# Optimization experiments

Measured on AMD Instinct MI355X. Metric: run time of the kernel, lower is better.

Reference implementation:

```python
import jax, jax.numpy as jnp
import numpy as np
from jax import lax

# Config (matches init_kwargs)
E = 8         # num_routed_experts
K = 2         # topk
D = 2048      # d_model
H = 1408      # moe_hidden_dimension
NS = 2        # num_shared_experts
B, T = 2, 2048
EPS = 1e-20   # topk_norm_epsilon
HS = H * NS   # shared expert hidden dim


def setup_inputs() -> dict:
    key = jax.random.key(0)
    ks = jax.random.split(key, 8)
    s = 0.02
    return {
        "x": jax.random.normal(ks[0], (B, T, D), jnp.float32),
        "router_w": jax.random.normal(ks[1], (E, D), jnp.float32) * 0.006,
        # routed experts, stacked: gate/up: [E, D, H], down: [E, H, D]
        "wg": jax.random.normal(ks[2], (E, D, H), jnp.float32) * s,
        "wu": jax.random.normal(ks[3], (E, D, H), jnp.float32) * s,
        "wd": jax.random.normal(ks[4], (E, H, D), jnp.float32) * s,
        # shared expert (single big SwiGLU FFN)
        "sg": jax.random.normal(ks[5], (D, HS), jnp.float32) * s,
        "su": jax.random.normal(ks[6], (D, HS), jnp.float32) * s,
        "sd": jax.random.normal(ks[7], (HS, D), jnp.float32) * s,
    }


def _silu(v):
    return v * jax.nn.sigmoid(v)


def reference(x, router_w, wg, wu, wd, sg, su, sd):
    b, t, d = x.shape
    xf = x.reshape(b * t, d)                       # [N, D]
    n = xf.shape[0]

    # Router: softmax over experts, then top-k masking (DeepSeek style)
    gates = jax.nn.softmax(xf @ router_w.T, axis=-1)           # [N, E]
    topv, topi = lax.top_k(gates, K)                           # [N, K]
    masked = jnp.zeros_like(gates).at[jnp.arange(n)[:, None], topi].set(topv)
    # normalized_moe_gates=True
    masked = masked / (masked.sum(axis=-1, keepdims=True) + EPS)  # [N, E]

    # Per-expert SwiGLU FFN, weighted-accumulated over experts.
    # Mathematically identical to gather/grouped-GEMM/scatter-add combine:
    # tokens with zero gate for expert e contribute 0.
    def step(acc, p):
        wg_e, wu_e, wd_e, g_e = p                  # g_e: [N] gate weights
        y = (_silu(xf @ wg_e) * (xf @ wu_e)) @ wd_e  # [N, D]
        return acc + y * g_e[:, None], None

    routed, _ = lax.scan(step, jnp.zeros_like(xf), (wg, wu, wd, masked.T))

    # Shared experts (dense path applied to every token)
    shared = (_silu(xf @ sg) * (xf @ su)) @ sd      # [N, D]

    return (routed + shared).reshape(b, t, d)
```

## Files before the change

kernel.cpp:

```cpp
#include <hip/hip_runtime.h>
#include <hip/hip_bf16.h>
#include <cstdint>

#define NTOK 4096
#define DMODEL 2048
#define NEXP 8
#define HR 1408
#define HSHARED 2816
#define MAXT64 136
#define MAXT128 72

typedef __attribute__((ext_vector_type(8))) short bf16x8;
typedef __attribute__((ext_vector_type(4))) float f32x4;

__device__ inline unsigned short f2b(float f) {
    unsigned u = __float_as_uint(f);
    u += 0x7fffu + ((u >> 16) & 1u);
    return (unsigned short)(u >> 16);
}
__device__ inline unsigned pack2(float a, float b) {
    return (unsigned)f2b(a) | ((unsigned)f2b(b) << 16);
}

__device__ __forceinline__ void gll16(unsigned short* lds, const unsigned short* g) {
    __builtin_amdgcn_global_load_lds(
        (__attribute__((address_space(1))) void*)g,
        (__attribute__((address_space(3))) void*)lds, 16, 0, 0);
}

__global__ __launch_bounds__(256) void k_router(const float* __restrict__ x,
                                                const float* __restrict__ rw,
                                                int* __restrict__ topi,
                                                float* __restrict__ topw,
                                                int* __restrict__ counts) {
    int gw = (blockIdx.x * 256 + threadIdx.x) >> 6;
    int lane = threadIdx.x & 63;
    if (gw >= NTOK) return;
    const float* xr = x + (size_t)gw * DMODEL;
    float s[NEXP] = {0.f,0.f,0.f,0.f,0.f,0.f,0.f,0.f};
    for (int d = lane; d < DMODEL; d += 64) {
        float xv = xr[d];
#pragma unroll
        for (int e = 0; e < NEXP; e++) s[e] = fmaf(xv, rw[e * DMODEL + d], s[e]);
    }
#pragma unroll
    for (int e = 0; e < NEXP; e++)
        for (int o = 32; o > 0; o >>= 1) s[e] += __shfl_xor(s[e], o, 64);
    if (lane == 0) {
        int i1 = 0;
#pragma unroll
        for (int e = 1; e < NEXP; e++) if (s[e] > s[i1]) i1 = e;
        int i2 = (i1 == 0) ? 1 : 0;
#pragma unroll
        for (int e = 0; e < NEXP; e++) if (e != i1 && s[e] > s[i2]) i2 = e;
        float mx = s[0];
#pragma unroll
        for (int e = 1; e < NEXP; e++) mx = fmaxf(mx, s[e]);
        float den = 0.f, ex[NEXP];
#pragma unroll
        for (int e = 0; e < NEXP; e++) { ex[e] = __expf(s[e] - mx); den += ex[e]; }
        float v1 = ex[i1] / den, v2 = ex[i2] / den;
        float inv = 1.f / (v1 + v2 + 1e-20f);
        topi[2 * gw] = i1; topi[2 * gw + 1] = i2;
        topw[2 * gw] = v1 * inv; topw[2 * gw + 1] = v2 * inv;
        atomicAdd(&counts[i1], 1); atomicAdd(&counts[i2], 1);
    }
}

__global__ void k_scan(int* counts, int* offsets, int* cursors, int* ntiles,
                       int* tile_e, int* tile_r, int step) {
    if (threadIdx.x == 0 && blockIdx.x == 0) {
        int off = 0, nt = 0;
        for (int e = 0; e < NEXP; e++) {
            offsets[e] = off; cursors[e] = off;
            int c = counts[e];
            for (int r = 0; r < c; r += step) { tile_e[nt] = e; tile_r[nt] = r; nt++; }
            off += c;
        }
        ntiles[0] = nt;
    }
}

__global__ __launch_bounds__(256) void k_fill(const int* __restrict__ topi,
                                              const float* __restrict__ topw,
                                              int* cursors, int* at, float* aw) {
    int t = blockIdx.x * 256 + threadIdx.x;
    if (t >= NTOK) return;
#pragma unroll
    for (int k = 0; k < 2; k++) {
        int e = topi[2 * t + k];
        int pos = atomicAdd(&cursors[e], 1);
        at[pos] = t; aw[pos] = topw[2 * t + k];
    }
}

__global__ __launch_bounds__(256) void k_cvt_x(const float* __restrict__ src,
                                               unsigned short* __restrict__ dst) {
    size_t i = ((size_t)blockIdx.x * 256 + threadIdx.x) * 8;
    float4 a = *(const float4*)(src + i);
    float4 b = *(const float4*)(src + i + 4);
    uint4 v; v.x = pack2(a.x, a.y); v.y = pack2(a.z, a.w);
    v.z = pack2(b.x, b.y); v.w = pack2(b.z, b.w);
    *(uint4*)(dst + i) = v;
}

__global__ __launch_bounds__(256) void k_tcvt(const float* __restrict__ src,
                                              unsigned short* __restrict__ dst,
                                              int K, int N) {
    src += (size_t)blockIdx.z * K * N;
    dst += (size_t)blockIdx.z * K * N;
    int n0 = blockIdx.x * 64, k0 = blockIdx.y * 64;
    __shared__ unsigned short T[64][72];
    int t = threadIdx.x;
    int kr = t >> 4, nc = (t & 15) * 4;
#pragma unroll
    for (int i = 0; i < 4; i++) {
        int k = kr + i * 16;
        float4 v = *(const float4*)(src + (size_t)(k0 + k) * N + n0 + nc);
        T[k][nc] = f2b(v.x); T[k][nc + 1] = f2b(v.y);
        T[k][nc + 2] = f2b(v.z); T[k][nc + 3] = f2b(v.w);
    }
    __syncthreads();
    int nr = t >> 3, kc = (t & 7) * 8;
#pragma unroll
    for (int j = 0; j < 2; j++) {
        int n = nr + j * 32;
        unsigned short tmp[8];
#pragma unroll
        for (int u = 0; u < 8; u++) tmp[u] = T[kc + u][n];
        *(uint4*)(dst + (size_t)(n0 + n) * K + k0 + kc) = *(uint4*)tmp;
    }
}


template <bool GATHERED>
__global__ __launch_bounds__(256) void kf_gateup(
    const unsigned short* __restrict__ xb, const unsigned short* __restrict__ BgT,
    const unsigned short* __restrict__ BuT, int K, int Hld, int ebase,
    const int* __restrict__ tile_e, const int* __restrict__ tile_r,
    const int* __restrict__ offsets, const int* __restrict__ counts,
    const int* __restrict__ ntiles, const int* __restrict__ at,
    unsigned short* __restrict__ hout) {
    int m0, mcnt;
    const unsigned short* bgw = BgT;
    const unsigned short* buw = BuT;
    if (GATHERED) {
        if ((int)blockIdx.x >= ntiles[0]) return;
        int e = tile_e[blockIdx.x];
        if (e < ebase || e >= ebase + 4) return;
        int ro = tile_r[blockIdx.x];
        m0 = offsets[e] + ro;
        mcnt = counts[e] - ro; if (mcnt > 128) mcnt = 128;
        size_t wofs = (size_t)(e - ebase) * Hld * K;
        bgw += wofs; buw += wofs;
    } else { m0 = blockIdx.x * 128; mcnt = 128; }
    int n0 = blockIdx.y * 64;

    __shared__ __align__(16) unsigned short As[128 * 64];
    __shared__ __align__(16) unsigned short Bgs[64 * 64];
    __shared__ __align__(16) unsigned short Bus[64 * 64];

    int tid = threadIdx.x;
    int wv = tid >> 6, lane = tid & 63;
    int rbase = tid >> 3;
    int kc = (tid & 7) ^ ((tid >> 3) & 7);
    const unsigned short* arp[4];
#pragma unroll
    for (int j = 0; j < 4; j++) {
        int row = j * 32 + rbase;
        int cl = row < mcnt ? row : mcnt - 1;
        int grow = GATHERED ? at[m0 + cl] : (m0 + cl);
        arp[j] = xb + (size_t)grow * K + kc * 8;
    }
    const unsigned short* bgp[2];
    const unsigned short* bup[2];
#pragma unroll
    for (int j = 0; j < 2; j++) {
        int row = j * 32 + rbase;
        bgp[j] = bgw + (size_t)(n0 + row) * K + kc * 8;
        bup[j] = buw + (size_t)(n0 + row) * K + kc * 8;
    }
    unsigned short* a_l = As + (wv << 6) * 8;
    unsigned short* g_l = Bgs + (wv << 6) * 8;
    unsigned short* u_l = Bus + (wv << 6) * 8;

    int fr = lane & 15, quad = lane >> 4, sw = fr & 7;
    int wm = (wv & 1) << 6, wn = (wv >> 1) << 5;

    f32x4 accg[4][2] = {};
    f32x4 accu[4][2] = {};

    for (int k0 = 0; k0 < K; k0 += 64) {
        __syncthreads();
#pragma unroll
        for (int j = 0; j < 4; j++) gll16(a_l + j * 2048, arp[j] + k0);
#pragma unroll
        for (int j = 0; j < 2; j++) {
            gll16(g_l + j * 2048, bgp[j] + k0);
            gll16(u_l + j * 2048, bup[j] + k0);
        }
        __syncthreads();
#pragma unroll
        for (int s = 0; s < 2; s++) {
            int off = (((s << 2) + quad) ^ sw) << 3;
            bf16x8 a[4], g[2], u[2];
#pragma unroll
            for (int tm = 0; tm < 4; tm++)
                a[tm] = *(const bf16x8*)&As[(wm + tm * 16 + fr) * 64 + off];
#pragma unroll
            for (int tn = 0; tn < 2; tn++) {
                int rb = (wn + tn * 16 + fr) * 64 + off;
                g[tn] = *(const bf16x8*)&Bgs[rb];
                u[tn] = *(const bf16x8*)&Bus[rb];
            }
#pragma unroll
            for (int tm = 0; tm < 4; tm++)
#pragma unroll
                for (int tn = 0; tn < 2; tn++) {
                    accg[tm][tn] = __builtin_amdgcn_mfma_f32_16x16x32_bf16(a[tm], g[tn], accg[tm][tn], 0, 0, 0);
                    accu[tm][tn] = __builtin_amdgcn_mfma_f32_16x16x32_bf16(a[tm], u[tn], accu[tm][tn], 0, 0, 0);
                }
        }
    }
#pragma unroll
    for (int tm = 0; tm < 4; tm++)
#pragma unroll
        for (int r = 0; r < 4; r++) {
            int row = wm + tm * 16 + (quad << 2) + r;
            if (row < mcnt) {
#pragma unroll
                for (int tn = 0; tn < 2; tn++) {
                    float gv = accg[tm][tn][r], uv = accu[tm][tn][r];
                    float hv = (gv / (1.f + __expf(-gv))) * uv;
                    hout[(size_t)(m0 + row) * Hld + n0 + wn + tn * 16 + fr] = f2b(hv);
                }
            }
        }
}

template <bool GATHERED>
__global__ __launch_bounds__(256) void kf_down(
    const unsigned short* __restrict__ h, const unsigned short* __restrict__ BT,
    int K,
    const int* __restrict__ tile_e, const int* __restrict__ tile_r,
    const int* __restrict__ offsets, const int* __restrict__ counts,
    const int* __restrict__ ntiles, const int* __restrict__ at,
    const float* __restrict__ awt, float* __restrict__ out) {
    int m0, mcnt;
    const unsigned short* bw = BT;
    if (GATHERED) {
        if ((int)blockIdx.x >= ntiles[0]) return;
        int e = tile_e[blockIdx.x], ro = tile_r[blockIdx.x];
        m0 = offsets[e] + ro;
        mcnt = counts[e] - ro; if (mcnt > 128) mcnt = 128;
        bw += (size_t)e * DMODEL * K;
    } else { m0 = blockIdx.x * 128; mcnt = 128; }
    int n0 = blockIdx.y * 128;

    __shared__ __align__(16) unsigned short As[128 * 64];
    __shared__ __align__(16) unsigned short Bs[128 * 64];

    int tid = threadIdx.x;
    int wv = tid >> 6, lane = tid & 63;
    int rbase = tid >> 3;
    int kc = (tid & 7) ^ ((tid >> 3) & 7);
    const unsigned short* arp[4];
    const unsigned short* brp[4];
#pragma unroll
    for (int j = 0; j < 4; j++) {
        int row = j * 32 + rbase;
        int cl = row < mcnt ? row : mcnt - 1;
        arp[j] = h + (size_t)(m0 + cl) * K + kc * 8;
        brp[j] = bw + (size_t)(n0 + row) * K + kc * 8;
    }
    unsigned short* a_l = As + (wv << 6) * 8;
    unsigned short* b_l = Bs + (wv << 6) * 8;

    int fr = lane & 15, quad = lane >> 4, sw = fr & 7;
    int wm = (wv & 1) << 6, wn = (wv >> 1) << 6;

    f32x4 acc[4][4] = {};

    for (int k0 = 0; k0 < K; k0 += 64) {
        __syncthreads();
#pragma unroll
        for (int j = 0; j < 4; j++) {
            gll16(a_l + j * 2048, arp[j] + k0);
            gll16(b_l + j * 2048, brp[j] + k0);
        }
        __syncthreads();
#pragma unroll
        for (int s = 0; s < 2; s++) {
            int off = (((s << 2) + quad) ^ sw) << 3;
            bf16x8 a[4], b[4];
#pragma unroll
            for (int tm = 0; tm < 4; tm++)
                a[tm] = *(const bf16x8*)&As[(wm + tm * 16 + fr) * 64 + off];
#pragma unroll
            for (int tn = 0; tn < 4; tn++)
                b[tn] = *(const bf16x8*)&Bs[(wn + tn * 16 + fr) * 64 + off];
#pragma unroll
            for (int tm = 0; tm < 4; tm++)
#pragma unroll
                for (int tn = 0; tn < 4; tn++)
                    acc[tm][tn] = __builtin_amdgcn_mfma_f32_16x16x32_bf16(a[tm], b[tn], acc[tm][tn], 0, 0, 0);
        }
    }
#pragma unroll
    for (int tm = 0; tm < 4; tm++)
#pragma unroll
        for (int r = 0; r < 4; r++) {
            int row = wm + tm * 16 + (quad << 2) + r;
            if (row < mcnt) {
                if (GATHERED) {
                    int tok = at[m0 + row];
                    float w = awt[m0 + row];
#pragma unroll
                    for (int tn = 0; tn < 4; tn++)
                        atomicAdd(&out[(size_t)tok * DMODEL + n0 + wn + tn * 16 + fr],
                                  w * acc[tm][tn][r]);
                } else {
#pragma unroll
                    for (int tn = 0; tn < 4; tn++)
                        out[(size_t)(m0 + row) * DMODEL + n0 + wn + tn * 16 + fr] =
                            acc[tm][tn][r];
                }
            }
        }
}

template <bool GATHERED>
__global__ __launch_bounds__(256) void k_gateup(
    const float* __restrict__ x, const float* __restrict__ Wg,
    const float* __restrict__ Wu, int Hld,
    const int* __restrict__ tile_e, const int* __restrict__ tile_r,
    const int* __restrict__ offsets, const int* __restrict__ counts,
    const int* __restrict__ ntiles, const int* __restrict__ at,
    unsigned short* __restrict__ hout) {
    int m0, mcnt;
    const float* wgp = Wg;
    const float* wup = Wu;
    if (GATHERED) {
        if ((int)blockIdx.x >= ntiles[0]) return;
        int e = tile_e[blockIdx.x], ro = tile_r[blockIdx.x];
        m0 = offsets[e] + ro;
        mcnt = counts[e] - ro; if (mcnt > 64) mcnt = 64;
        size_t wofs = (size_t)e * DMODEL * Hld;
        wgp += wofs; wup += wofs;
    } else { m0 = blockIdx.x * 64; mcnt = 64; }
    int n0 = blockIdx.y * 64;
    __shared__ unsigned short As[64][48];
    __shared__ unsigned short Bgs[64][48];
    __shared__ unsigned short Bus[64][48];
    int tid = threadIdx.x;
    int ai = tid >> 2, ak = (tid & 3) << 3;
    int arowi = m0 + (ai < mcnt ? ai : (mcnt - 1));
    const float* arow = x + (size_t)(GATHERED ? at[arowi] : arowi) * DMODEL;
    int bn = tid >> 2, bk = (tid & 3) << 1;
    const float* bcolg = wgp + (size_t)n0 + bn;
    const float* bcolu = wup + (size_t)n0 + bn;
    int lane = tid & 63, wv = tid >> 6;
    int wm = (wv & 1) << 5, wn = (wv >> 1) << 5;
    int fr = lane & 15, fk = (lane >> 4) << 3;
    f32x4 accg[2][2] = {};
    f32x4 accu[2][2] = {};
    for (int k0 = 0; k0 < DMODEL; k0 += 32) {
        __syncthreads();
        float4 a0 = *(const float4*)(arow + k0 + ak);
        float4 a1 = *(const float4*)(arow + k0 + ak + 4);
        uint4 av; av.x = pack2(a0.x, a0.y); av.y = pack2(a0.z, a0.w);
        av.z = pack2(a1.x, a1.y); av.w = pack2(a1.z, a1.w);
        *(uint4*)&As[ai][ak] = av;
#pragma unroll
        for (int j = 0; j < 4; j++) {
            int kk = bk + (j << 3);
            size_t o0 = (size_t)(k0 + kk) * Hld;
            *(unsigned*)&Bgs[bn][kk] = pack2(bcolg[o0], bcolg[o0 + Hld]);
            *(unsigned*)&Bus[bn][kk] = pack2(bcolu[o0], bcolu[o0 + Hld]);
        }
        __syncthreads();
        bf16x8 af[2], bg[2], bu[2];
#pragma unroll
        for (int t = 0; t < 2; t++) {
            af[t] = *(bf16x8*)&As[wm + t * 16 + fr][fk];
            bg[t] = *(bf16x8*)&Bgs[wn + t * 16 + fr][fk];
            bu[t] = *(bf16x8*)&Bus[wn + t * 16 + fr][fk];
        }
#pragma unroll
        for (int tm = 0; tm < 2; tm++)
#pragma unroll
            for (int tn = 0; tn < 2; tn++) {
                accg[tm][tn] = __builtin_amdgcn_mfma_f32_16x16x32_bf16(af[tm], bg[tn], accg[tm][tn], 0, 0, 0);
                accu[tm][tn] = __builtin_amdgcn_mfma_f32_16x16x32_bf16(af[tm], bu[tn], accu[tm][tn], 0, 0, 0);
            }
    }
    int quad = (lane >> 4) << 2;
#pragma unroll
    for (int tm = 0; tm < 2; tm++)
#pragma unroll
        for (int r = 0; r < 4; r++) {
            int row = wm + tm * 16 + quad + r;
            if (row < mcnt) {
#pragma unroll
                for (int tn = 0; tn < 2; tn++) {
                    float g = accg[tm][tn][r], u = accu[tm][tn][r];
                    float hv = (g / (1.f + __expf(-g))) * u;
                    hout[(size_t)(m0 + row) * Hld + n0 + wn + tn * 16 + fr] = f2b(hv);
                }
            }
        }
}

template <bool GATHERED>
__global__ __launch_bounds__(256) void k_down(
    const unsigned short* __restrict__ h, const float* __restrict__ Wd, int Hld,
    const int* __restrict__ tile_e, const int* __restrict__ tile_r,
    const int* __restrict__ offsets, const int* __restrict__ counts,
    const int* __restrict__ ntiles, const int* __restrict__ at,
    const float* __restrict__ aw, float* __restrict__ out) {
    int m0, mcnt;
    const float* wdp = Wd;
    if (GATHERED) {
        if ((int)blockIdx.x >= ntiles[0]) return;
        int e = tile_e[blockIdx.x], ro = tile_r[blockIdx.x];
        m0 = offsets[e] + ro;
        mcnt = counts[e] - ro; if (mcnt > 64) mcnt = 64;
        wdp += (size_t)e * Hld * DMODEL;
    } else { m0 = blockIdx.x * 64; mcnt = 64; }
    int n0 = blockIdx.y * 64;
    __shared__ unsigned short As[64][48];
    __shared__ unsigned short Bs[64][48];
    int tid = threadIdx.x;
    int ai = tid >> 2, ak = (tid & 3) << 3;
    const unsigned short* arow = h + (size_t)(m0 + (ai < mcnt ? ai : (mcnt - 1))) * Hld;
    int bn = tid >> 2, bk = (tid & 3) << 1;
    const float* bcol = wdp + (size_t)n0 + bn;
    int lane = tid & 63, wv = tid >> 6;
    int wm = (wv & 1) << 5, wn = (wv >> 1) << 5;
    int fr = lane & 15, fk = (lane >> 4) << 3;
    f32x4 acc[2][2] = {};
    for (int k0 = 0; k0 < Hld; k0 += 32) {
        __syncthreads();
        *(uint4*)&As[ai][ak] = *(const uint4*)(arow + k0 + ak);
#pragma unroll
        for (int j = 0; j < 4; j++) {
            int kk = bk + (j << 3);
            size_t o0 = (size_t)(k0 + kk) * DMODEL;
            *(unsigned*)&Bs[bn][kk] = pack2(bcol[o0], bcol[o0 + DMODEL]);
        }
        __syncthreads();
        bf16x8 af[2], bf[2];
#pragma unroll
        for (int t = 0; t < 2; t++) {
            af[t] = *(bf16x8*)&As[wm + t * 16 + fr][fk];
            bf[t] = *(bf16x8*)&Bs[wn + t * 16 + fr][fk];
        }
#pragma unroll
        for (int tm = 0; tm < 2; tm++)
#pragma unroll
            for (int tn = 0; tn < 2; tn++)
                acc[tm][tn] = __builtin_amdgcn_mfma_f32_16x16x32_bf16(af[tm], bf[tn], acc[tm][tn], 0, 0, 0);
    }
    int quad = (lane >> 4) << 2;
#pragma unroll
    for (int tm = 0; tm < 2; tm++)
#pragma unroll
        for (int r = 0; r < 4; r++) {
            int row = wm + tm * 16 + quad + r;
            if (row < mcnt) {
                int mrow = m0 + row;
                int tok = GATHERED ? at[mrow] : mrow;
                float w = GATHERED ? aw[mrow] : 1.f;
#pragma unroll
                for (int tn = 0; tn < 2; tn++)
                    atomicAdd(&out[(size_t)tok * DMODEL + n0 + wn + tn * 16 + fr],
                              w * acc[tm][tn][r]);
            }
        }
}

extern "C" void kernel_launch(void* const* d_in, const int* in_sizes, int n_in,
                              void* d_out, int out_size, void* d_ws, size_t ws_size,
                              hipStream_t stream) {
    (void)in_sizes; (void)n_in;
    const float* x  = (const float*)d_in[0];
    const float* rw = (const float*)d_in[1];
    const float* wg = (const float*)d_in[2];
    const float* wu = (const float*)d_in[3];
    const float* wd = (const float*)d_in[4];
    const float* sg = (const float*)d_in[5];
    const float* su = (const float*)d_in[6];
    const float* sd = (const float*)d_in[7];
    float* out = (float*)d_out;

    int* counts  = (int*)d_ws;
    int* offsets = counts + 8;
    int* cursors = counts + 16;
    int* ntiles  = counts + 24;
    int* tile_e  = counts + 32;
    int* tile_r  = tile_e + 144;
    int* topi    = tile_r + 144;
    float* topw  = (float*)(topi + 8192);
    int* at      = (int*)(topw + 8192);
    float* aw    = (float*)(at + 8192);

    const size_t META = 262144;
    const size_t XB   = (size_t)NTOK * DMODEL * 2;
    const size_t POOL_NEED = 69206016;
    const size_t FAST_NEED = META + XB + POOL_NEED;
    bool fast = ws_size >= FAST_NEED;

    hipMemsetAsync(counts, 0, 32, stream);
    k_router<<<dim3(NTOK / 4), 256, 0, stream>>>(x, rw, topi, topw, counts);
    k_scan<<<1, 64, 0, stream>>>(counts, offsets, cursors, ntiles, tile_e, tile_r,
                                 fast ? 128 : 64);
    k_fill<<<dim3(NTOK / 256), 256, 0, stream>>>(topi, topw, cursors, at, aw);

    if (fast) {
        char* base = (char*)d_ws;
        unsigned short* xb = (unsigned short*)(base + META);
        char* pool = base + META + XB;
        unsigned short* sgT = (unsigned short*)pool;
        unsigned short* suT = (unsigned short*)(pool + 11534336);
        unsigned short* h_s = (unsigned short*)(pool + 23068672);
        unsigned short* sdT = (unsigned short*)(pool + 46137344);
        unsigned short* wgT = (unsigned short*)pool;
        unsigned short* wuT = (unsigned short*)(pool + 23068672);
        unsigned short* h_r = (unsigned short*)(pool + 46137344);
        unsigned short* wdT = (unsigned short*)pool;

        k_cvt_x<<<dim3(4096), 256, 0, stream>>>(x, xb);

        k_tcvt<<<dim3(HSHARED / 64, DMODEL / 64, 1), 256, 0, stream>>>(sg, sgT, DMODEL, HSHARED);
        k_tcvt<<<dim3(HSHARED / 64, DMODEL / 64, 1), 256, 0, stream>>>(su, suT, DMODEL, HSHARED);
        kf_gateup<false><<<dim3(NTOK / 128, HSHARED / 64), 256, 0, stream>>>(
            xb, sgT, suT, DMODEL, HSHARED, 0,
            nullptr, nullptr, nullptr, nullptr, nullptr, nullptr, h_s);
        k_tcvt<<<dim3(DMODEL / 64, HSHARED / 64, 1), 256, 0, stream>>>(sd, sdT, HSHARED, DMODEL);
        kf_down<false><<<dim3(NTOK / 128, DMODEL / 128), 256, 0, stream>>>(
            h_s, sdT, HSHARED,
            nullptr, nullptr, nullptr, nullptr, nullptr, nullptr, nullptr, out);

        k_tcvt<<<dim3(HR / 64, DMODEL / 64, 4), 256, 0, stream>>>(wg, wgT, DMODEL, HR);
        k_tcvt<<<dim3(HR / 64, DMODEL / 64, 4), 256, 0, stream>>>(wu, wuT, DMODEL, HR);
        kf_gateup<true><<<dim3(MAXT128, HR / 64), 256, 0, stream>>>(
            xb, wgT, wuT, DMODEL, HR, 0,
            tile_e, tile_r, offsets, counts, ntiles, at, h_r);
        k_tcvt<<<dim3(HR / 64, DMODEL / 64, 4), 256, 0, stream>>>(
            wg + (size_t)4 * DMODEL * HR, wgT, DMODEL, HR);
        k_tcvt<<<dim3(HR / 64, DMODEL / 64, 4), 256, 0, stream>>>(
            wu + (size_t)4 * DMODEL * HR, wuT, DMODEL, HR);
        kf_gateup<true><<<dim3(MAXT128, HR / 64), 256, 0, stream>>>(
            xb, wgT, wuT, DMODEL, HR, 4,
            tile_e, tile_r, offsets, counts, ntiles, at, h_r);
        k_tcvt<<<dim3(DMODEL / 64, HR / 64, 8), 256, 0, stream>>>(wd, wdT, HR, DMODEL);
        kf_down<true><<<dim3(MAXT128, DMODEL / 128), 256, 0, stream>>>(
            h_r, wdT, HR,
            tile_e, tile_r, offsets, counts, ntiles, at, aw, out);
    } else {
        unsigned short* h_r =
            (unsigned short*)(((uintptr_t)(aw + 8192) + 255) & ~(uintptr_t)255);
        unsigned short* h_s = h_r + (size_t)8192 * HR;
        hipMemsetAsync(out, 0, (size_t)out_size * sizeof(float), stream);
        k_gateup<true><<<dim3(MAXT64, HR / 64), 256, 0, stream>>>(
            x, wg, wu, HR, tile_e, tile_r, offsets, counts, ntiles, at, h_r);
        k_gateup<false><<<dim3(NTOK / 64, HSHARED / 64), 256, 0, stream>>>(
            x, sg, su, HSHARED, nullptr, nullptr, nullptr, nullptr, nullptr, nullptr, h_s);
        k_down<true><<<dim3(MAXT64, DMODEL / 64), 256, 0, stream>>>(
            h_r, wd, HR, tile_e, tile_r, offsets, counts, ntiles, at, aw, out);
        k_down<false><<<dim3(NTOK / 64, DMODEL / 64), 256, 0, stream>>>(
            h_s, sd, HSHARED, nullptr, nullptr, nullptr, nullptr, nullptr, nullptr, nullptr, out);
    }
}
```

Baseline: 965.8 us.

## Merge shared and routed expert GEMMs into single grouped launches, fuse x conversion into router

After: 968.5 us. No clear change (+0.3%).

```diff
diff --git a/kernel.cpp b/kernel.cpp
--- a/kernel.cpp
+++ b/kernel.cpp
@@ -7,7 +7,6 @@
 #define NEXP 8
 #define HR 1408
 #define HSHARED 2816
-#define MAXT64 136
 #define MAXT128 72
 
 typedef __attribute__((ext_vector_type(8))) short bf16x8;
@@ -28,42 +27,60 @@
         (__attribute__((address_space(3))) void*)lds, 16, 0, 0);
 }
 
-__global__ __launch_bounds__(256) void k_router(const float* __restrict__ x,
-                                                const float* __restrict__ rw,
-                                                int* __restrict__ topi,
-                                                float* __restrict__ topw,
-                                                int* __restrict__ counts) {
-    int gw = (blockIdx.x * 256 + threadIdx.x) >> 6;
-    int lane = threadIdx.x & 63;
-    if (gw >= NTOK) return;
-    const float* xr = x + (size_t)gw * DMODEL;
-    float s[NEXP] = {0.f,0.f,0.f,0.f,0.f,0.f,0.f,0.f};
-    for (int d = lane; d < DMODEL; d += 64) {
-        float xv = xr[d];
-#pragma unroll
-        for (int e = 0; e < NEXP; e++) s[e] = fmaf(xv, rw[e * DMODEL + d], s[e]);
-    }
-#pragma unroll
-    for (int e = 0; e < NEXP; e++)
-        for (int o = 32; o > 0; o >>= 1) s[e] += __shfl_xor(s[e], o, 64);
-    if (lane == 0) {
-        int i1 = 0;
-#pragma unroll
-        for (int e = 1; e < NEXP; e++) if (s[e] > s[i1]) i1 = e;
-        int i2 = (i1 == 0) ? 1 : 0;
-#pragma unroll
-        for (int e = 0; e < NEXP; e++) if (e != i1 && s[e] > s[i2]) i2 = e;
-        float mx = s[0];
-#pragma unroll
-        for (int e = 1; e < NEXP; e++) mx = fmaxf(mx, s[e]);
-        float den = 0.f, ex[NEXP];
-#pragma unroll
-        for (int e = 0; e < NEXP; e++) { ex[e] = __expf(s[e] - mx); den += ex[e]; }
-        float v1 = ex[i1] / den, v2 = ex[i2] / den;
-        float inv = 1.f / (v1 + v2 + 1e-20f);
-        topi[2 * gw] = i1; topi[2 * gw + 1] = i2;
-        topw[2 * gw] = v1 * inv; topw[2 * gw + 1] = v2 * inv;
-        atomicAdd(&counts[i1], 1); atomicAdd(&counts[i2], 1);
+__global__ __launch_bounds__(256) void k_router2(const float* __restrict__ x,
+                                                 const float* __restrict__ rw,
+                                                 unsigned short* __restrict__ xb,
+                                                 int* __restrict__ topi,
+                                                 float* __restrict__ topw,
+                                                 int* __restrict__ counts) {
+    __shared__ float rws[NEXP * DMODEL];
+    int tid = threadIdx.x;
+    for (int i = tid * 4; i < NEXP * DMODEL; i += 1024)
+        *(float4*)&rws[i] = *(const float4*)&rw[i];
+    __syncthreads();
+    int wv = tid >> 6, lane = tid & 63;
+#pragma unroll
+    for (int tk = 0; tk < 2; tk++) {
+        int tok = blockIdx.x * 8 + wv * 2 + tk;
+        const float* xr = x + (size_t)tok * DMODEL;
+        unsigned short* xbr = xb + (size_t)tok * DMODEL;
+        float s[NEXP] = {0.f,0.f,0.f,0.f,0.f,0.f,0.f,0.f};
+#pragma unroll
+        for (int i = 0; i < 8; i++) {
+            int d = i * 256 + lane * 4;
+            float4 xv = *(const float4*)(xr + d);
+            uint2 p; p.x = pack2(xv.x, xv.y); p.y = pack2(xv.z, xv.w);
+            *(uint2*)(xbr + d) = p;
+#pragma unroll
+            for (int e = 0; e < NEXP; e++) {
+                float4 w = *(const float4*)&rws[e * DMODEL + d];
+                s[e] = fmaf(xv.x, w.x, s[e]); s[e] = fmaf(xv.y, w.y, s[e]);
+                s[e] = fmaf(xv.z, w.z, s[e]); s[e] = fmaf(xv.w, w.w, s[e]);
+            }
+        }
+#pragma unroll
+        for (int e = 0; e < NEXP; e++)
+#pragma unroll
+            for (int o = 32; o > 0; o >>= 1) s[e] += __shfl_xor(s[e], o, 64);
+        if (lane == 0) {
+            int i1 = 0;
+#pragma unroll
+            for (int e = 1; e < NEXP; e++) if (s[e] > s[i1]) i1 = e;
+            int i2 = (i1 == 0) ? 1 : 0;
+#pragma unroll
+            for (int e = 0; e < NEXP; e++) if (e != i1 && s[e] > s[i2]) i2 = e;
+            float mx = s[0];
+#pragma unroll
+            for (int e = 1; e < NEXP; e++) mx = fmaxf(mx, s[e]);
+            float den = 0.f, ex[NEXP];
+#pragma unroll
+            for (int e = 0; e < NEXP; e++) { ex[e] = __expf(s[e] - mx); den += ex[e]; }
+            float v1 = ex[i1] / den, v2 = ex[i2] / den;
+            float inv = 1.f / (v1 + v2 + 1e-20f);
+            topi[2 * tok] = i1; topi[2 * tok + 1] = i2;
+            topw[2 * tok] = v1 * inv; topw[2 * tok + 1] = v2 * inv;
+            atomicAdd(&counts[i1], 1); atomicAdd(&counts[i2], 1);
+        }
     }
 }
 
@@ -94,22 +111,9 @@
     }
 }
 
-__global__ __launch_bounds__(256) void k_cvt_x(const float* __restrict__ src,
-                                               unsigned short* __restrict__ dst) {
-    size_t i = ((size_t)blockIdx.x * 256 + threadIdx.x) * 8;
-    float4 a = *(const float4*)(src + i);
-    float4 b = *(const float4*)(src + i + 4);
-    uint4 v; v.x = pack2(a.x, a.y); v.y = pack2(a.z, a.w);
-    v.z = pack2(b.x, b.y); v.w = pack2(b.z, b.w);
-    *(uint4*)(dst + i) = v;
-}
-
-__global__ __launch_bounds__(256) void k_tcvt(const float* __restrict__ src,
-                                              unsigned short* __restrict__ dst,
-                                              int K, int N) {
-    src += (size_t)blockIdx.z * K * N;
-    dst += (size_t)blockIdx.z * K * N;
-    int n0 = blockIdx.x * 64, k0 = blockIdx.y * 64;
+__device__ __forceinline__ void tcvt_tile(const float* __restrict__ src,
+                                          unsigned short* __restrict__ dst,
+                                          int N, int dstride, int n0, int k0) {
     __shared__ unsigned short T[64][72];
     int t = threadIdx.x;
     int kr = t >> 4, nc = (t & 15) * 4;
@@ -128,10 +132,259 @@
         unsigned short tmp[8];
 #pragma unroll
         for (int u = 0; u < 8; u++) tmp[u] = T[kc + u][n];
-        *(uint4*)(dst + (size_t)(n0 + n) * K + k0 + kc) = *(uint4*)tmp;
-    }
-}
-
+        *(uint4*)(dst + (size_t)(n0 + n) * dstride + k0 + kc) = *(uint4*)tmp;
+    }
+}
+
+__global__ __launch_bounds__(256) void k_tcvt_gu(const float* __restrict__ wg,
+                                                 const float* __restrict__ wu,
+                                                 unsigned short* __restrict__ wgT,
+                                                 unsigned short* __restrict__ wuT) {
+    int z = blockIdx.z;
+    const float* src = (z < 8 ? wg : wu) + (size_t)(z & 7) * DMODEL * HR;
+    unsigned short* dst = (z < 8 ? wgT : wuT) + (size_t)(z & 7) * HR * DMODEL;
+    tcvt_tile(src, dst, HR, DMODEL, blockIdx.x * 64, blockIdx.y * 64);
+}
+
+__global__ __launch_bounds__(256) void k_tcvt_s(const float* __restrict__ sg,
+                                                const float* __restrict__ su,
+                                                unsigned short* __restrict__ sgT,
+                                                unsigned short* __restrict__ suT) {
+    int z = blockIdx.z;
+    tcvt_tile(z ? su : sg, z ? suT : sgT, HSHARED, DMODEL,
+              blockIdx.x * 64, blockIdx.y * 64);
+}
+
+__global__ __launch_bounds__(256) void k_tcvt_d(const float* __restrict__ wd,
+                                                const float* __restrict__ sd,
+                                                unsigned short* __restrict__ wdT,
+                                                unsigned short* __restrict__ sdT) {
+    int z = blockIdx.z;
+    const float* src;
+    unsigned short* dst;
+    int dstride;
+    if (z < 8) {
+        src = wd + (size_t)z * HR * DMODEL;
+        dst = wdT + (size_t)z * DMODEL * HR;
+        dstride = HR;
+    } else {
+        src = sd + (size_t)(z - 8) * HR * DMODEL;
+        dst = sdT + (size_t)(z - 8) * HR;
+        dstride = HSHARED;
+    }
+    tcvt_tile(src, dst, DMODEL, dstride, blockIdx.x * 64, blockIdx.y * 64);
+}
+
+#define GU_SH_JOBS 1408
+#define GU_RT_NB   22
+__global__ __launch_bounds__(256) void kg_all(
+    const unsigned short* __restrict__ xb,
+    const unsigned short* __restrict__ sgT, const unsigned short* __restrict__ suT,
+    const unsigned short* __restrict__ wgT, const unsigned short* __restrict__ wuT,
+    const int* __restrict__ tile_e, const int* __restrict__ tile_r,
+    const int* __restrict__ offsets, const int* __restrict__ counts,
+    const int* __restrict__ ntiles, const int* __restrict__ at,
+    unsigned short* __restrict__ h_s, unsigned short* __restrict__ h_r) {
+    int j = blockIdx.x;
+    int m0, mcnt, n0, Hld;
+    const unsigned short *Bg, *Bu;
+    unsigned short* ho;
+    bool gath;
+    if (j < GU_SH_JOBS) {
+        gath = false;
+        m0 = (j / 44) * 128; mcnt = 128;
+        n0 = (j % 44) * 64;
+        Bg = sgT; Bu = suT; Hld = HSHARED; ho = h_s;
+    } else {
+        j -= GU_SH_JOBS;
+        int tile = j / GU_RT_NB;
+        if (tile >= ntiles[0]) return;
+        gath = true;
+        n0 = (j % GU_RT_NB) * 64;
+        int e = tile_e[tile], ro = tile_r[tile];
+        m0 = offsets[e] + ro;
+        mcnt = counts[e] - ro; if (mcnt > 128) mcnt = 128;
+        size_t wo = (size_t)e * HR * DMODEL;
+        Bg = wgT + wo; Bu = wuT + wo; Hld = HR; ho = h_r;
+    }
+
+    __shared__ __align__(16) unsigned short As[128 * 64];
+    __shared__ __align__(16) unsigned short Bgs[64 * 64];
+    __shared__ __align__(16) unsigned short Bus[64 * 64];
+
+    int tid = threadIdx.x;
+    int wv = tid >> 6, lane = tid & 63;
+    int rbase = tid >> 3;
+    int kc = (tid & 7) ^ ((tid >> 3) & 7);
+    const unsigned short* arp[4];
+#pragma unroll
+    for (int j2 = 0; j2 < 4; j2++) {
+        int row = j2 * 32 + rbase;
+        int cl = row < mcnt ? row : mcnt - 1;
+        int grow = gath ? at[m0 + cl] : (m0 + cl);
+        arp[j2] = xb + (size_t)grow * DMODEL + kc * 8;
+    }
+    const unsigned short* bgp[2];
+    const unsigned short* bup[2];
+#pragma unroll
+    for (int j2 = 0; j2 < 2; j2++) {
+        int row = j2 * 32 + rbase;
+        bgp[j2] = Bg + (size_t)(n0 + row) * DMODEL + kc * 8;
+        bup[j2] = Bu + (size_t)(n0 + row) * DMODEL + kc * 8;
+    }
+    unsigned short* a_l = As + (wv << 6) * 8;
+    unsigned short* g_l = Bgs + (wv << 6) * 8;
+    unsigned short* u_l = Bus + (wv << 6) * 8;
+
+    int fr = lane & 15, quad = lane >> 4, sw = fr & 7;
+    int wm = (wv & 1) << 6, wn = (wv >> 1) << 5;
+
+    f32x4 accg[4][2] = {};
+    f32x4 accu[4][2] = {};
+
+    for (int k0 = 0; k0 < DMODEL; k0 += 64) {
+        __syncthreads();
+#pragma unroll
+        for (int j2 = 0; j2 < 4; j2++) gll16(a_l + j2 * 2048, arp[j2] + k0);
+#pragma unroll
+        for (int j2 = 0; j2 < 2; j2++) {
+            gll16(g_l + j2 * 2048, bgp[j2] + k0);
+            gll16(u_l + j2 * 2048, bup[j2] + k0);
+        }
+        __syncthreads();
+#pragma unroll
+        for (int s = 0; s < 2; s++) {
+            int off = (((s << 2) + quad) ^ sw) << 3;
+            bf16x8 a[4], g[2], u[2];
+#pragma unroll
+            for (int tm = 0; tm < 4; tm++)
+                a[tm] = *(const bf16x8*)&As[(wm + tm * 16 + fr) * 64 + off];
+#pragma unroll
+            for (int tn = 0; tn < 2; tn++) {
+                int rb = (wn + tn * 16 + fr) * 64 + off;
+                g[tn] = *(const bf16x8*)&Bgs[rb];
+                u[tn] = *(const bf16x8*)&Bus[rb];
+            }
+#pragma unroll
+            for (int tm = 0; tm < 4; tm++)
+#pragma unroll
+                for (int tn = 0; tn < 2; tn++) {
+                    accg[tm][tn] = __builtin_amdgcn_mfma_f32_16x16x32_bf16(a[tm], g[tn], accg[tm][tn], 0, 0, 0);
+                    accu[tm][tn] = __builtin_amdgcn_mfma_f32_16x16x32_bf16(a[tm], u[tn], accu[tm][tn], 0, 0, 0);
+                }
+        }
+    }
+#pragma unroll
+    for (int tm = 0; tm < 4; tm++)
+#pragma unroll
+        for (int r = 0; r < 4; r++) {
+            int row = wm + tm * 16 + (quad << 2) + r;
+            if (row < mcnt) {
+#pragma unroll
+                for (int tn = 0; tn < 2; tn++) {
+                    float gv = accg[tm][tn][r], uv = accu[tm][tn][r];
+                    float hv = (gv / (1.f + __expf(-gv))) * uv;
+                    ho[(size_t)(m0 + row) * Hld + n0 + wn + tn * 16 + fr] = f2b(hv);
+                }
+            }
+        }
+}
+
+#define DN_SH_JOBS 512
+__global__ __launch_bounds__(256) void kd_all(
+    const unsigned short* __restrict__ h_s, const unsigned short* __restrict__ h_r,
+    const unsigned short* __restrict__ sdT, const unsigned short* __restrict__ wdT,
+    const int* __restrict__ tile_e, const int* __restrict__ tile_r,
+    const int* __restrict__ offsets, const int* __restrict__ counts,
+    const int* __restrict__ ntiles, const int* __restrict__ at,
+    const float* __restrict__ aw, float* __restrict__ out) {
+    int j = blockIdx.x;
+    int m0, mcnt, n0, Kd;
+    const unsigned short *Ab, *Bb;
+    bool gath;
+    if (j < DN_SH_JOBS) {
+        gath = false;
+        m0 = (j >> 4) * 128; mcnt = 128;
+        n0 = (j & 15) * 128;
+        Ab = h_s; Bb = sdT; Kd = HSHARED;
+    } else {
+        j -= DN_SH_JOBS;
+        int tile = j >> 4;
+        if (tile >= ntiles[0]) return;
+        gath = true;
+        n0 = (j & 15) * 128;
+        int e = tile_e[tile], ro = tile_r[tile];
+        m0 = offsets[e] + ro;
+        mcnt = counts[e] - ro; if (mcnt > 128) mcnt = 128;
+        Ab = h_r; Bb = wdT + (size_t)e * DMODEL * HR;
+        Kd = HR;
+    }
+
+    __shared__ __align__(16) unsigned short As[128 * 64];
+    __shared__ __align__(16) unsigned short Bs[128 * 64];
+
+    int tid = threadIdx.x;
+    int wv = tid >> 6, lane = tid & 63;
+    int rbase = tid >> 3;
+    int kc = (tid & 7) ^ ((tid >> 3) & 7);
+    const unsigned short* arp[4];
+    const unsigned short* brp[4];
+#pragma unroll
+    for (int j2 = 0; j2 < 4; j2++) {
+        int row = j2 * 32 + rbase;
+        int cl = row < mcnt ? row : mcnt - 1;
+        arp[j2] = Ab + (size_t)(m0 + cl) * Kd + kc * 8;
+        brp[j2] = Bb + (size_t)(n0 + row) * Kd + kc * 8;
+    }
+    unsigned short* a_l = As + (wv << 6) * 8;
+    unsigned short* b_l = Bs + (wv << 6) * 8;
+
+    int fr = lane & 15, quad = lane >> 4, sw = fr & 7;
+    int wm = (wv & 1) << 6, wn = (wv >> 1) << 6;
+
+    f32x4 acc[4][4] = {};
+
+    for (int k0 = 0; k0 < Kd; k0 += 64) {
+        __syncthreads();
+#pragma unroll
+        for (int j2 = 0; j2 < 4; j2++) {
+            gll16(a_l + j2 * 2048, arp[j2] + k0);
+            gll16(b_l + j2 * 2048, brp[j2] + k0);
+        }
+        __syncthreads();
+#pragma unroll
+        for (int s = 0; s < 2; s++) {
+            int off = (((s << 2) + quad) ^ sw) << 3;
+            bf16x8 a[4], b[4];
+#pragma unroll
+            for (int tm = 0; tm < 4; tm++)
+                a[tm] = *(const bf16x8*)&As[(wm + tm * 16 + fr) * 64 + off];
+#pragma unroll
+            for (int tn = 0; tn < 4; tn++)
+                b[tn] = *(const bf16x8*)&Bs[(wn + tn * 16 + fr) * 64 + off];
+#pragma unroll
+            for (int tm = 0; tm < 4; tm++)
+#pragma unroll
+                for (int tn = 0; tn < 4; tn++)
+                    acc[tm][tn] = __builtin_amdgcn_mfma_f32_16x16x32_bf16(a[tm], b[tn], acc[tm][tn], 0, 0, 0);
+        }
+    }
+#pragma unroll
+    for (int tm = 0; tm < 4; tm++)
+#pragma unroll
+        for (int r = 0; r < 4; r++) {
+            int row = wm + tm * 16 + (quad << 2) + r;
+            if (row < mcnt) {
+                int tok; float w;
+                if (gath) { tok = at[m0 + row]; w = aw[m0 + row]; }
+                else      { tok = m0 + row;     w = 1.f; }
+#pragma unroll
+                for (int tn = 0; tn < 4; tn++)
+                    atomicAdd(&out[(size_t)tok * DMODEL + n0 + wn + tn * 16 + fr],
+                              w * acc[tm][tn][r]);
+            }
+        }
+}
 
 template <bool GATHERED>
 __global__ __launch_bounds__(256) void kf_gateup(
@@ -155,11 +408,9 @@
         bgw += wofs; buw += wofs;
     } else { m0 = blockIdx.x * 128; mcnt = 128; }
     int n0 = blockIdx.y * 64;
-
     __shared__ __align__(16) unsigned short As[128 * 64];
     __shared__ __align__(16) unsigned short Bgs[64 * 64];
     __shared__ __align__(16) unsigned short Bus[64 * 64];
-
     int tid = threadIdx.x;
     int wv = tid >> 6, lane = tid & 63;
     int rbase = tid >> 3;
@@ -183,13 +434,10 @@
     unsigned short* a_l = As + (wv << 6) * 8;
     unsigned short* g_l = Bgs + (wv << 6) * 8;
     unsigned short* u_l = Bus + (wv << 6) * 8;
-
     int fr = lane & 15, quad = lane >> 4, sw = fr & 7;
     int wm = (wv & 1) << 6, wn = (wv >> 1) << 5;
-
     f32x4 accg[4][2] = {};
     f32x4 accu[4][2] = {};
-
     for (int k0 = 0; k0 < K; k0 += 64) {
         __syncthreads();
 #pragma unroll
@@ -256,10 +504,8 @@
         bw += (size_t)e * DMODEL * K;
     } else { m0 = blockIdx.x * 128; mcnt = 128; }
     int n0 = blockIdx.y * 128;
-
     __shared__ __align__(16) unsigned short As[128 * 64];
     __shared__ __align__(16) unsigned short Bs[128 * 64];
-
     int tid = threadIdx.x;
     int wv = tid >> 6, lane = tid & 63;
     int rbase = tid >> 3;
@@ -275,12 +521,9 @@
     }
     unsigned short* a_l = As + (wv << 6) * 8;
     unsigned short* b_l = Bs + (wv << 6) * 8;
-
     int fr = lane & 15, quad = lane >> 4, sw = fr & 7;
     int wm = (wv & 1) << 6, wn = (wv >> 1) << 6;
-
     f32x4 acc[4][4] = {};
-
     for (int k0 = 0; k0 < K; k0 += 64) {
         __syncthreads();
 #pragma unroll
@@ -329,154 +572,12 @@
         }
 }
 
-template <bool GATHERED>
-__global__ __launch_bounds__(256) void k_gateup(
-    const float* __restrict__ x, const float* __restrict__ Wg,
-    const float* __restrict__ Wu, int Hld,
-    const int* __restrict__ tile_e, const int* __restrict__ tile_r,
-    const int* __restrict__ offsets, const int* __restrict__ counts,
-    const int* __restrict__ ntiles, const int* __restrict__ at,
-    unsigned short* __restrict__ hout) {
-    int m0, mcnt;
-    const float* wgp = Wg;
-    const float* wup = Wu;
-    if (GATHERED) {
-        if ((int)blockIdx.x >= ntiles[0]) return;
-        int e = tile_e[blockIdx.x], ro = tile_r[blockIdx.x];
-        m0 = offsets[e] + ro;
-        mcnt = counts[e] - ro; if (mcnt > 64) mcnt = 64;
-        size_t wofs = (size_t)e * DMODEL * Hld;
-        wgp += wofs; wup += wofs;
-    } else { m0 = blockIdx.x * 64; mcnt = 64; }
-    int n0 = blockIdx.y * 64;
-    __shared__ unsigned short As[64][48];
-    __shared__ unsigned short Bgs[64][48];
-    __shared__ unsigned short Bus[64][48];
-    int tid = threadIdx.x;
-    int ai = tid >> 2, ak = (tid & 3) << 3;
-    int arowi = m0 + (ai < mcnt ? ai : (mcnt - 1));
-    const float* arow = x + (size_t)(GATHERED ? at[arowi] : arowi) * DMODEL;
-    int bn = tid >> 2, bk = (tid & 3) << 1;
-    const float* bcolg = wgp + (size_t)n0 + bn;
-    const float* bcolu = wup + (size_t)n0 + bn;
-    int lane = tid & 63, wv = tid >> 6;
-    int wm = (wv & 1) << 5, wn = (wv >> 1) << 5;
-    int fr = lane & 15, fk = (lane >> 4) << 3;
-    f32x4 accg[2][2] = {};
-    f32x4 accu[2][2] = {};
-    for (int k0 = 0; k0 < DMODEL; k0 += 32) {
-        __syncthreads();
-        float4 a0 = *(const float4*)(arow + k0 + ak);
-        float4 a1 = *(const float4*)(arow + k0 + ak + 4);
-        uint4 av; av.x = pack2(a0.x, a0.y); av.y = pack2(a0.z, a0.w);
-        av.z = pack2(a1.x, a1.y); av.w = pack2(a1.z, a1.w);
-        *(uint4*)&As[ai][ak] = av;
-#pragma unroll
-        for (int j = 0; j < 4; j++) {
-            int kk = bk + (j << 3);
-            size_t o0 = (size_t)(k0 + kk) * Hld;
-            *(unsigned*)&Bgs[bn][kk] = pack2(bcolg[o0], bcolg[o0 + Hld]);
-            *(unsigned*)&Bus[bn][kk] = pack2(bcolu[o0], bcolu[o0 + Hld]);
-        }
-        __syncthreads();
-        bf16x8 af[2], bg[2], bu[2];
-#pragma unroll
-        for (int t = 0; t < 2; t++) {
-            af[t] = *(bf16x8*)&As[wm + t * 16 + fr][fk];
-            bg[t] = *(bf16x8*)&Bgs[wn + t * 16 + fr][fk];
-            bu[t] = *(bf16x8*)&Bus[wn + t * 16 + fr][fk];
-        }
-#pragma unroll
-        for (int tm = 0; tm < 2; tm++)
-#pragma unroll
-            for (int tn = 0; tn < 2; tn++) {
-                accg[tm][tn] = __builtin_amdgcn_mfma_f32_16x16x32_bf16(af[tm], bg[tn], accg[tm][tn], 0, 0, 0);
-                accu[tm][tn] = __builtin_amdgcn_mfma_f32_16x16x32_bf16(af[tm], bu[tn], accu[tm][tn], 0, 0, 0);
-            }
-    }
-    int quad = (lane >> 4) << 2;
-#pragma unroll
-    for (int tm = 0; tm < 2; tm++)
-#pragma unroll
-        for (int r = 0; r < 4; r++) {
-            int row = wm + tm * 16 + quad + r;
-            if (row < mcnt) {
-#pragma unroll
-                for (int tn = 0; tn < 2; tn++) {
-                    float g = accg[tm][tn][r], u = accu[tm][tn][r];
-                    float hv = (g / (1.f + __expf(-g))) * u;
-                    hout[(size_t)(m0 + row) * Hld + n0 + wn + tn * 16 + fr] = f2b(hv);
-                }
-            }
-        }
-}
-
-template <bool GATHERED>
-__global__ __launch_bounds__(256) void k_down(
-    const unsigned short* __restrict__ h, const float* __restrict__ Wd, int Hld,
-    const int* __restrict__ tile_e, const int* __restrict__ tile_r,
-    const int* __restrict__ offsets, const int* __restrict__ counts,
-    const int* __restrict__ ntiles, const int* __restrict__ at,
-    const float* __restrict__ aw, float* __restrict__ out) {
-    int m0, mcnt;
-    const float* wdp = Wd;
-    if (GATHERED) {
-        if ((int)blockIdx.x >= ntiles[0]) return;
-        int e = tile_e[blockIdx.x], ro = tile_r[blockIdx.x];
-        m0 = offsets[e] + ro;
-        mcnt = counts[e] - ro; if (mcnt > 64) mcnt = 64;
-        wdp += (size_t)e * Hld * DMODEL;
-    } else { m0 = blockIdx.x * 64; mcnt = 64; }
-    int n0 = blockIdx.y * 64;
-    __shared__ unsigned short As[64][48];
-    __shared__ unsigned short Bs[64][48];
-    int tid = threadIdx.x;
-    int ai = tid >> 2, ak = (tid & 3) << 3;
-    const unsigned short* arow = h + (size_t)(m0 + (ai < mcnt ? ai : (mcnt - 1))) * Hld;
-    int bn = tid >> 2, bk = (tid & 3) << 1;
-    const float* bcol = wdp + (size_t)n0 + bn;
-    int lane = tid & 63, wv = tid >> 6;
-    int wm = (wv & 1) << 5, wn = (wv >> 1) << 5;
-    int fr = lane & 15, fk = (lane >> 4) << 3;
-    f32x4 acc[2][2] = {};
-    for (int k0 = 0; k0 < Hld; k0 += 32) {
-        __syncthreads();
-        *(uint4*)&As[ai][ak] = *(const uint4*)(arow + k0 + ak);
-#pragma unroll
-        for (int j = 0; j < 4; j++) {
-            int kk = bk + (j << 3);
-            size_t o0 = (size_t)(k0 + kk) * DMODEL;
-            *(unsigned*)&Bs[bn][kk] = pack2(bcol[o0], bcol[o0 + DMODEL]);
-        }
-        __syncthreads();
-        bf16x8 af[2], bf[2];
-#pragma unroll
-        for (int t = 0; t < 2; t++) {
-            af[t] = *(bf16x8*)&As[wm + t * 16 + fr][fk];
-            bf[t] = *(bf16x8*)&Bs[wn + t * 16 + fr][fk];
-        }
-#pragma unroll
-        for (int tm = 0; tm < 2; tm++)
-#pragma unroll
-            for (int tn = 0; tn < 2; tn++)
-                acc[tm][tn] = __builtin_amdgcn_mfma_f32_16x16x32_bf16(af[tm], bf[tn], acc[tm][tn], 0, 0, 0);
-    }
-    int quad = (lane >> 4) << 2;
-#pragma unroll
-    for (int tm = 0; tm < 2; tm++)
-#pragma unroll
-        for (int r = 0; r < 4; r++) {
-            int row = wm + tm * 16 + quad + r;
-            if (row < mcnt) {
-                int mrow = m0 + row;
-                int tok = GATHERED ? at[mrow] : mrow;
-                float w = GATHERED ? aw[mrow] : 1.f;
-#pragma unroll
-                for (int tn = 0; tn < 2; tn++)
-                    atomicAdd(&out[(size_t)tok * DMODEL + n0 + wn + tn * 16 + fr],
-                              w * acc[tm][tn][r]);
-            }
-        }
+__global__ __launch_bounds__(256) void k_tcvt(const float* __restrict__ src,
+                                              unsigned short* __restrict__ dst,
+                                              int K, int N) {
+    src += (size_t)blockIdx.z * K * N;
+    dst += (size_t)blockIdx.z * K * N;
+    tcvt_tile(src, dst, N, K, blockIdx.x * 64, blockIdx.y * 64);
 }
 
 extern "C" void kernel_launch(void* const* d_in, const int* in_sizes, int n_in,
@@ -506,20 +607,38 @@
 
     const size_t META = 262144;
     const size_t XB   = (size_t)NTOK * DMODEL * 2;
-    const size_t POOL_NEED = 69206016;
-    const size_t FAST_NEED = META + XB + POOL_NEED;
-    bool fast = ws_size >= FAST_NEED;
+    unsigned short* xb = (unsigned short*)((char*)d_ws + META);
+
+    const size_t FULL_NEED = 178520064;
+    const size_t FAST_NEED = 86245376;
 
     hipMemsetAsync(counts, 0, 32, stream);
-    k_router<<<dim3(NTOK / 4), 256, 0, stream>>>(x, rw, topi, topw, counts);
-    k_scan<<<1, 64, 0, stream>>>(counts, offsets, cursors, ntiles, tile_e, tile_r,
-                                 fast ? 128 : 64);
+    k_router2<<<dim3(512), 256, 0, stream>>>(x, rw, xb, topi, topw, counts);
+    k_scan<<<1, 64, 0, stream>>>(counts, offsets, cursors, ntiles, tile_e, tile_r, 128);
     k_fill<<<dim3(NTOK / 256), 256, 0, stream>>>(topi, topw, cursors, at, aw);
 
-    if (fast) {
-        char* base = (char*)d_ws;
-        unsigned short* xb = (unsigned short*)(base + META);
-        char* pool = base + META + XB;
+    if (ws_size >= FULL_NEED) {
+        char* pool = (char*)d_ws + META + XB;
+        unsigned short* wgT = (unsigned short*)pool;
+        unsigned short* wuT = (unsigned short*)(pool + 46137344);
+        unsigned short* sgT = (unsigned short*)(pool + 92274688);
+        unsigned short* suT = (unsigned short*)(pool + 103809024);
+        unsigned short* wdT = (unsigned short*)pool;
+        unsigned short* sdT = (unsigned short*)(pool + 46137344);
+        unsigned short* h_r = (unsigned short*)(pool + 115343360);
+        unsigned short* h_s = h_r + (size_t)8192 * HR;
+
+        hipMemsetAsync(out, 0, (size_t)out_size * sizeof(float), stream);
+        k_tcvt_gu<<<dim3(22, 32, 16), 256, 0, stream>>>(wg, wu, wgT, wuT);
+        k_tcvt_s<<<dim3(44, 32, 2), 256, 0, stream>>>(sg, su, sgT, suT);
+        kg_all<<<dim3(GU_SH_JOBS + MAXT128 * GU_RT_NB), 256, 0, stream>>>(
+            xb, sgT, suT, wgT, wuT, tile_e, tile_r, offsets, counts, ntiles, at,
+            h_s, h_r);
+        k_tcvt_d<<<dim3(32, 22, 10), 256, 0, stream>>>(wd, sd, wdT, sdT);
+        kd_all<<<dim3(DN_SH_JOBS + MAXT128 * 16), 256, 0, stream>>>(
+            h_s, h_r, sdT, wdT, tile_e, tile_r, offsets, counts, ntiles, at, aw, out);
+    } else {
+        char* pool = (char*)d_ws + META + XB;
         unsigned short* sgT = (unsigned short*)pool;
         unsigned short* suT = (unsigned short*)(pool + 11534336);
         unsigned short* h_s = (unsigned short*)(pool + 23068672);
@@ -528,8 +647,6 @@
         unsigned short* wuT = (unsigned short*)(pool + 23068672);
         unsigned short* h_r = (unsigned short*)(pool + 46137344);
         unsigned short* wdT = (unsigned short*)pool;
-
-        k_cvt_x<<<dim3(4096), 256, 0, stream>>>(x, xb);
 
         k_tcvt<<<dim3(HSHARED / 64, DMODEL / 64, 1), 256, 0, stream>>>(sg, sgT, DMODEL, HSHARED);
         k_tcvt<<<dim3(HSHARED / 64, DMODEL / 64, 1), 256, 0, stream>>>(su, suT, DMODEL, HSHARED);
@@ -540,7 +657,6 @@
         kf_down<false><<<dim3(NTOK / 128, DMODEL / 128), 256, 0, stream>>>(
             h_s, sdT, HSHARED,
             nullptr, nullptr, nullptr, nullptr, nullptr, nullptr, nullptr, out);
-
         k_tcvt<<<dim3(HR / 64, DMODEL / 64, 4), 256, 0, stream>>>(wg, wgT, DMODEL, HR);
         k_tcvt<<<dim3(HR / 64, DMODEL / 64, 4), 256, 0, stream>>>(wu, wuT, DMODEL, HR);
         kf_gateup<true><<<dim3(MAXT128, HR / 64), 256, 0, stream>>>(
@@ -557,18 +673,5 @@
         kf_down<true><<<dim3(MAXT128, DMODEL / 128), 256, 0, stream>>>(
             h_r, wdT, HR,
             tile_e, tile_r, offsets, counts, ntiles, at, aw, out);
-    } else {
-        unsigned short* h_r =
-            (unsigned short*)(((uintptr_t)(aw + 8192) + 255) & ~(uintptr_t)255);
-        unsigned short* h_s = h_r + (size_t)8192 * HR;
-        hipMemsetAsync(out, 0, (size_t)out_size * sizeof(float), stream);
-        k_gateup<true><<<dim3(MAXT64, HR / 64), 256, 0, stream>>>(
-            x, wg, wu, HR, tile_e, tile_r, offsets, counts, ntiles, at, h_r);
-        k_gateup<false><<<dim3(NTOK / 64, HSHARED / 64), 256, 0, stream>>>(
-            x, sg, su, HSHARED, nullptr, nullptr, nullptr, nullptr, nullptr, nullptr, h_s);
-        k_down<true><<<dim3(MAXT64, DMODEL / 64), 256, 0, stream>>>(
-            h_r, wd, HR, tile_e, tile_r, offsets, counts, ntiles, at, aw, out);
-        k_down<false><<<dim3(NTOK / 64, DMODEL / 64), 256, 0, stream>>>(
-            h_s, sd, HSHARED, nullptr, nullptr, nullptr, nullptr, nullptr, nullptr, nullptr, out);
-    }
-}
+    }
+}
```
